# Kernel optimization log

Hardware: AMD Instinct MI355X
Metric: run time of the kernel (lower is better)

Reference implementation:

```python
import jax, jax.numpy as jnp
import numpy as np

B, S, HID = 16, 1024, 768
H, DH = 12, HID // 12


def setup_inputs() -> dict:
    key = jax.random.key(0)
    ks = jax.random.split(key, 10)
    scale = 1.0 / np.sqrt(HID)
    return {
        "hidden_states": jax.random.normal(ks[0], (B, S, HID), jnp.float32),
        "Wq": jax.random.normal(ks[1], (HID, HID), jnp.float32) * scale,
        "bq": jnp.zeros((HID,), jnp.float32),
        "Wk": jax.random.normal(ks[2], (HID, HID), jnp.float32) * scale,
        "bk": jnp.zeros((HID,), jnp.float32),
        "Wv": jax.random.normal(ks[3], (HID, HID), jnp.float32) * scale,
        "bv": jnp.zeros((HID,), jnp.float32),
        # torch init is zeros; use small randn so the linear-attention correction term is exercised
        "phi_k": jax.random.normal(ks[4], (1, H, DH, 1), jnp.float32) * 0.02,
        "phi_kv": jax.random.normal(ks[5], (1, H, DH, DH), jnp.float32) * 0.02,
    }


def _heads(x):
    # [B,S,HID] -> [B,H,S,DH]
    return x.reshape(B, S, H, DH).transpose(0, 2, 1, 3)


def reference(hidden_states, Wq, bq, Wk, bk, Wv, bv, phi_k, phi_kv):
    q = _heads(hidden_states @ Wq.T + bq)
    k = _heads(hidden_states @ Wk.T + bk)
    v = _heads(hidden_states @ Wv.T + bv)

    # phi(x) = ELU(x / d^0.25) + 1   (dropout disabled: eval-mode reference)
    phi_q = jax.nn.elu(q / jnp.asarray(DH, jnp.float32) ** 0.25) + 1.0

    # full softmax-style attention scores with max-subtract
    A = jnp.einsum("bhsd,bhtd->bhst", q, k) / jnp.sqrt(jnp.asarray(DH, jnp.float32))
    max_A = jnp.max(A, axis=-1, keepdims=True)          # [B,H,S,1]
    exp_max_A = jnp.exp(max_A)
    A = jnp.exp(A - max_A)                              # [B,H,S,S]

    # custom normalizer: softmax mass + linear-attention correction
    D = jnp.sum(A, axis=-1, keepdims=True) + jnp.matmul(phi_q, jnp.abs(phi_k)) / exp_max_A

    ctx = (jnp.matmul(A, v) + jnp.matmul(phi_q, phi_kv) / exp_max_A) / D  # [B,H,S,DH]
    out = ctx.transpose(0, 2, 1, 3).reshape(B, S, HID)
    return out
```

## Files before the change

### kernel.cpp

```cpp
#include <hip/hip_runtime.h>
#include <cstdint>
#include <cstddef>

typedef _Float16 f16x8 __attribute__((ext_vector_type(8)));
typedef _Float16 f16x4 __attribute__((ext_vector_type(4)));
typedef float    f32x4 __attribute__((ext_vector_type(4)));
typedef unsigned u32;
typedef const u32 __attribute__((address_space(1)))* gas_ptr;
typedef u32 __attribute__((address_space(3)))* las_ptr;

#define MFMA16(a, b, c) __builtin_amdgcn_mfma_f32_16x16x32_f16((a), (b), (c), 0, 0, 0)

static constexpr int Bb   = 16;
static constexpr int Ss   = 1024;
static constexpr int HID  = 768;
static constexpr int Hh   = 12;
static constexpr int DH   = 64;
static constexpr int Mrows = Bb * Ss;
static constexpr int N3    = 3 * HID;

static constexpr float QSCL  = 0.125f * 1.44269504088896f;
static constexpr float PHSCL = 1.9605161f;

__global__ void prep(const float* __restrict__ hs, _Float16* __restrict__ A16,
                     const float* __restrict__ Wq, const float* __restrict__ Wk,
                     const float* __restrict__ Wv, const float* __restrict__ bq,
                     const float* __restrict__ bk, const float* __restrict__ bv,
                     _Float16* __restrict__ Wt, float* __restrict__ bias) {
    const int i = blockIdx.x * 256 + threadIdx.x;
    if (i < Mrows * HID / 4) {
        float4 v = ((const float4*)hs)[i];
        f16x4 o;
        o[0] = (_Float16)v.x; o[1] = (_Float16)v.y;
        o[2] = (_Float16)v.z; o[3] = (_Float16)v.w;
        ((f16x4*)A16)[i] = o;
    }
    if (i < N3 * HID / 8) {
        const int i8 = i * 8;
        int n = i8 / HID;
        int k = i8 - n * HID;
        int sel = n / HID;
        int nn  = n - sel * HID;
        const float* W = (sel == 0) ? Wq : (sel == 1) ? Wk : Wv;
        const float* wp = W + (size_t)nn * HID + k;
        float4 v0 = *(const float4*)wp;
        float4 v1 = *(const float4*)(wp + 4);
        uint4 o;
        o.x = __builtin_bit_cast(u32, __builtin_amdgcn_cvt_pkrtz(v0.x, v0.y));
        o.y = __builtin_bit_cast(u32, __builtin_amdgcn_cvt_pkrtz(v0.z, v0.w));
        o.z = __builtin_bit_cast(u32, __builtin_amdgcn_cvt_pkrtz(v1.x, v1.y));
        o.w = __builtin_bit_cast(u32, __builtin_amdgcn_cvt_pkrtz(v1.z, v1.w));
        *(uint4*)(Wt + i8) = o;
    }
    if (i < N3) {
        int wsel = i / HID, j = i - wsel * HID;
        bias[i] = (wsel == 0) ? bq[j] : (wsel == 1) ? bk[j] : bv[j];
    }
}

__global__ __launch_bounds__(256, 2) void qkv_gemm(
    const _Float16* __restrict__ A, const _Float16* __restrict__ Bt,
    const float* __restrict__ bias,
    _Float16* __restrict__ Qo, _Float16* __restrict__ Ko, _Float16* __restrict__ VTo) {
    __shared__ _Float16 As[2][128 * 32];
    __shared__ _Float16 Bs[2][128 * 32];
    const int tid  = threadIdx.x;
    const int lane = tid & 63, wid = tid >> 6;
    const int g = lane >> 4, c = lane & 15;
    const int bm = blockIdx.x & 127, bn = blockIdx.x >> 7;
    const int m0 = bm * 128, n0 = bn * 128;
    const int wm = wid >> 1, wn = wid & 1;

    f32x4 acc[4][4] = {};

    auto stage = [&](int bf, int kt) {
#pragma unroll
        for (int i = 0; i < 2; ++i) {
            int ch  = i * 256 + wid * 64 + lane;
            int row = ch >> 2;
            int kh  = ((ch & 3) ^ ((row >> 1) & 3)) << 3;
            __builtin_amdgcn_global_load_lds(
                (gas_ptr)(A + (size_t)(m0 + row) * HID + kt + kh),
                (las_ptr)(&As[bf][(i * 256 + wid * 64) * 8]), 16, 0, 0);
            __builtin_amdgcn_global_load_lds(
                (gas_ptr)(Bt + (size_t)(n0 + row) * HID + kt + kh),
                (las_ptr)(&Bs[bf][(i * 256 + wid * 64) * 8]), 16, 0, 0);
        }
    };

    stage(0, 0);
    __syncthreads();

    for (int kt = 0; kt < HID; kt += 32) {
        const int cur = (kt >> 5) & 1;
        if (kt + 32 < HID) stage(cur ^ 1, kt + 32);

        f16x8 af[4], bf[4];
#pragma unroll
        for (int mi = 0; mi < 4; ++mi) {
            const int row = wm * 64 + mi * 16 + c;
            af[mi] = *(const f16x8*)((const char*)&As[cur][0] + row * 64 + ((g ^ ((row >> 1) & 3)) << 4));
        }
#pragma unroll
        for (int ni = 0; ni < 4; ++ni) {
            const int row = wn * 64 + ni * 16 + c;
            bf[ni] = *(const f16x8*)((const char*)&Bs[cur][0] + row * 64 + ((g ^ ((row >> 1) & 3)) << 4));
        }
#pragma unroll
        for (int mi = 0; mi < 4; ++mi)
#pragma unroll
            for (int ni = 0; ni < 4; ++ni)
                acc[mi][ni] = MFMA16(af[mi], bf[ni], acc[mi][ni]);

        __syncthreads();
    }

#pragma unroll
    for (int ni = 0; ni < 4; ++ni) {
        const int col    = n0 + wn * 64 + ni * 16 + c;
        const int which  = col / HID;
        const int within = col - which * HID;
        const int hh = within >> 6, d = within & 63;
        const float bias_v = bias[col];
        const float scl = (which == 0) ? QSCL : 1.0f;
#pragma unroll
        for (int mi = 0; mi < 4; ++mi) {
            const int rowg0 = m0 + wm * 64 + mi * 16 + g * 4;
            const int bidx = rowg0 >> 10, s0 = rowg0 & 1023;
            const int bh   = bidx * Hh + hh;
            f16x4 hv4;
#pragma unroll
            for (int r = 0; r < 4; ++r)
                hv4[r] = (_Float16)((acc[mi][ni][r] + bias_v) * scl);
            if (which == 2) {
                const int base64 = (m0 + wm * 64) & 1023;
                const int p = 32 * (mi >> 1) + 8 * g + 4 * (mi & 1);
                *(uint2*)(VTo + ((size_t)bh * DH + d) * Ss + base64 + p) = __builtin_bit_cast(uint2, hv4);
            } else if (which == 0) {
#pragma unroll
                for (int r = 0; r < 4; ++r)
                    Qo[((size_t)bh * Ss + s0 + r) * DH + d] = hv4[r];
            } else {
#pragma unroll
                for (int r = 0; r < 4; ++r)
                    Ko[((size_t)bh * Ss + s0 + r) * DH + d] = hv4[r];
            }
        }
    }
}

__global__ __launch_bounds__(256) void attn_kernel(
    const _Float16* __restrict__ Q, const _Float16* __restrict__ K,
    const _Float16* __restrict__ VT, const float* __restrict__ phi_k,
    const float* __restrict__ phi_kv, float* __restrict__ out) {
    __shared__ _Float16 Kb[2][64 * 64];
    __shared__ _Float16 Vb[2][64 * 64];

    const int tid  = threadIdx.x;
    const int lane = tid & 63, w = tid >> 6;
    const int g = lane >> 4, c = lane & 15;

    const int wg = (blockIdx.x & 7) * 192 + (blockIdx.x >> 3);
    const int bh = wg >> 3, qt = wg & 7;
    const int b = bh / Hh, h = bh - b * Hh;
    const size_t base = (size_t)bh * Ss * DH;
    const _Float16* Kg = K + base;
    const _Float16* Vg = VT + base;

    const int srow = lane >> 3;
    const int scol = (((lane & 7) ^ srow) << 4) >> 1;
    const int sw = (c & 7) << 4;

    const _Float16* Qp = Q + base + (size_t)(qt * 128 + w * 32 + c) * DH + g * 8;
    f16x8 aq[2][2];
    aq[0][0] = *(const f16x8*)(Qp);
    aq[0][1] = *(const f16x8*)(Qp + 32);
    aq[1][0] = *(const f16x8*)(Qp + 16 * DH);
    aq[1][1] = *(const f16x8*)(Qp + 16 * DH + 32);

    float part[2] = {0.f, 0.f};
    f32x4 acco[2][4] = {};

    auto stage = [&](int bf, int t0) {
#pragma unroll
        for (int i = 0; i < 2; ++i) {
            const int row0 = w * 16 + i * 8;
            __builtin_amdgcn_global_load_lds(
                (gas_ptr)(Kg + (size_t)(t0 + row0 + srow) * DH + scol),
                (las_ptr)(&Kb[bf][row0 * 64]), 16, 0, 0);
            __builtin_amdgcn_global_load_lds(
                (gas_ptr)(Vg + (size_t)(row0 + srow) * Ss + t0 + scol),
                (las_ptr)(&Vb[bf][row0 * 64]), 16, 0, 0);
        }
    };

    stage(0, 0);
    __syncthreads();

    for (int t0 = 0; t0 < Ss; t0 += 64) {
        const int bf = (t0 >> 6) & 1;
        if (t0 + 64 < Ss) stage(bf ^ 1, t0 + 64);

        f32x4 z[2][4];
        __builtin_amdgcn_s_setprio(1);
#pragma unroll
        for (int nt = 0; nt < 4; ++nt) {
            const char* kb = (const char*)&Kb[bf][0] + (nt * 16 + c) * 128;
            f16x8 bk0 = *(const f16x8*)(kb + ((g * 16) ^ sw));
            f16x8 bk1 = *(const f16x8*)(kb + ((64 + g * 16) ^ sw));
            f32x4 z0 = {}, z1 = {};
            z0 = MFMA16(bk0, aq[0][0], z0);
            z0 = MFMA16(bk1, aq[0][1], z0);
            z1 = MFMA16(bk0, aq[1][0], z1);
            z1 = MFMA16(bk1, aq[1][1], z1);
            z[0][nt] = z0;
            z[1][nt] = z1;
        }
        __builtin_amdgcn_s_setprio(0);

        f16x8 pb[2][2];
#pragma unroll
        for (int mb = 0; mb < 2; ++mb) {
#pragma unroll
            for (int kk = 0; kk < 2; ++kk) {
                float e0 = __builtin_amdgcn_exp2f(z[mb][2 * kk][0]);
                float e1 = __builtin_amdgcn_exp2f(z[mb][2 * kk][1]);
                float e2 = __builtin_amdgcn_exp2f(z[mb][2 * kk][2]);
                float e3 = __builtin_amdgcn_exp2f(z[mb][2 * kk][3]);
                float e4 = __builtin_amdgcn_exp2f(z[mb][2 * kk + 1][0]);
                float e5 = __builtin_amdgcn_exp2f(z[mb][2 * kk + 1][1]);
                float e6 = __builtin_amdgcn_exp2f(z[mb][2 * kk + 1][2]);
                float e7 = __builtin_amdgcn_exp2f(z[mb][2 * kk + 1][3]);
                part[mb] += (e0 + e1 + e2 + e3) + (e4 + e5 + e6 + e7);
                uint4 pk;
                pk.x = __builtin_bit_cast(u32, __builtin_amdgcn_cvt_pkrtz(e0, e1));
                pk.y = __builtin_bit_cast(u32, __builtin_amdgcn_cvt_pkrtz(e2, e3));
                pk.z = __builtin_bit_cast(u32, __builtin_amdgcn_cvt_pkrtz(e4, e5));
                pk.w = __builtin_bit_cast(u32, __builtin_amdgcn_cvt_pkrtz(e6, e7));
                pb[mb][kk] = __builtin_bit_cast(f16x8, pk);
            }
        }

        __builtin_amdgcn_s_setprio(1);
#pragma unroll
        for (int nd = 0; nd < 4; ++nd) {
            const char* vb = (const char*)&Vb[bf][0] + (nd * 16 + c) * 128;
#pragma unroll
            for (int kk = 0; kk < 2; ++kk) {
                f16x8 va = *(const f16x8*)(vb + ((kk * 64 + g * 16) ^ sw));
                acco[0][nd] = MFMA16(va, pb[0][kk], acco[0][nd]);
                acco[1][nd] = MFMA16(va, pb[1][kk], acco[1][nd]);
            }
        }
        __builtin_amdgcn_s_setprio(0);
        __syncthreads();
    }

    const float* phk = phi_k + h * DH;
    const float* pkv = phi_kv + h * DH * DH;

    f16x8 pq2[2][2];
    float invD[2];
#pragma unroll
    for (int mb = 0; mb < 2; ++mb) {
        const _Float16* Qr = Q + base + (size_t)(qt * 128 + w * 32 + mb * 16 + c) * DH;
        float dot = 0.f;
#pragma unroll
        for (int kk = 0; kk < 2; ++kk) {
            f16x4 qa = *(const f16x4*)(Qr + kk * 32 + 4 * g);
            f16x4 qb = *(const f16x4*)(Qr + kk * 32 + 16 + 4 * g);
            float4 fka = *(const float4*)(phk + kk * 32 + 4 * g);
            float4 fkb = *(const float4*)(phk + kk * 32 + 16 + 4 * g);
            const float fa[4] = {fka.x, fka.y, fka.z, fka.w};
            const float fb[4] = {fkb.x, fkb.y, fkb.z, fkb.w};
            f16x8 pq;
#pragma unroll
            for (int j = 0; j < 4; ++j) {
                float x0 = (float)qa[j] * PHSCL;
                float x1 = (float)qb[j] * PHSCL;
                float p0 = (x0 > 0.f) ? (x0 + 1.f) : __expf(x0);
                float p1 = (x1 > 0.f) ? (x1 + 1.f) : __expf(x1);
                dot += p0 * fabsf(fa[j]) + p1 * fabsf(fb[j]);
                pq[j]     = (_Float16)p0;
                pq[4 + j] = (_Float16)p1;
            }
            pq2[mb][kk] = pq;
        }
        dot += __shfl_xor(dot, 16);
        dot += __shfl_xor(dot, 32);
        float s = part[mb];
        s += __shfl_xor(s, 16);
        s += __shfl_xor(s, 32);
        invD[mb] = 1.f / (s + dot);
    }

#pragma unroll
    for (int nd = 0; nd < 4; ++nd) {
        f16x8 fa[2];
#pragma unroll
        for (int kk = 0; kk < 2; ++kk) {
            f16x8 t;
#pragma unroll
            for (int j = 0; j < 8; ++j) {
                int dh = kk * 32 + 16 * (j >> 2) + 4 * g + (j & 3);
                t[j] = (_Float16)pkv[dh * DH + nd * 16 + c];
            }
            fa[kk] = t;
        }
#pragma unroll
        for (int mb = 0; mb < 2; ++mb) {
            f32x4 cc = {};
            cc = MFMA16(fa[0], pq2[mb][0], cc);
            cc = MFMA16(fa[1], pq2[mb][1], cc);
            f32x4 o = (acco[mb][nd] + cc) * invD[mb];
            const int srow_o = qt * 128 + w * 32 + mb * 16 + c;
            float* op = out + ((size_t)b * Ss + srow_o) * HID + h * DH + nd * 16 + 4 * g;
            *(f32x4*)op = o;
        }
    }
}

extern "C" void kernel_launch(void* const* d_in, const int* in_sizes, int n_in,
                              void* d_out, int out_size, void* d_ws, size_t ws_size,
                              hipStream_t stream) {
    (void)in_sizes; (void)n_in; (void)out_size;
    const float* hs   = (const float*)d_in[0];
    const float* Wq   = (const float*)d_in[1];
    const float* bq   = (const float*)d_in[2];
    const float* Wk   = (const float*)d_in[3];
    const float* bk   = (const float*)d_in[4];
    const float* Wv   = (const float*)d_in[5];
    const float* bv   = (const float*)d_in[6];
    const float* phik = (const float*)d_in[7];
    const float* phikv= (const float*)d_in[8];
    float* out = (float*)d_out;

    char* ws = (char*)d_ws;
    constexpr size_t szA   = (size_t)Mrows * HID * 2;
    constexpr size_t szWt  = (size_t)N3 * HID * 2;
    constexpr size_t szBia = (size_t)N3 * 4;
    constexpr size_t szQ   = (size_t)Bb * Hh * Ss * DH * 2;
    _Float16* A16  = (_Float16*)(ws);
    _Float16* Wt   = (_Float16*)(ws + szA);
    float*    bias = (float*)(ws + szA + szWt);
    _Float16* Qb   = (_Float16*)(ws + szA + szWt + szBia);
    _Float16* Kb   = (_Float16*)(ws + szA + szWt + szBia + szQ);
    _Float16* VTb  = (_Float16*)(ws + szA + szWt + szBia + 2 * szQ);
    (void)ws_size;

    prep<<<(Mrows * HID / 4 + 255) / 256, 256, 0, stream>>>(hs, A16, Wq, Wk, Wv, bq, bk, bv, Wt, bias);
    qkv_gemm<<<dim3((Mrows / 128) * (N3 / 128)), 256, 0, stream>>>(A16, Wt, bias, Qb, Kb, VTb);
    attn_kernel<<<dim3(Bb * Hh * (Ss / 128)), 256, 0, stream>>>(Qb, Kb, VTb, phik, phikv, out);
}
```

Baseline: 178.2 us.

## Replace double-buffered K=32 QKV GEMM staging with single-buffer K=64 tiles

```diff
diff --git a/kernel.cpp b/kernel.cpp
--- a/kernel.cpp
+++ b/kernel.cpp
@@ -62,8 +62,8 @@
     const _Float16* __restrict__ A, const _Float16* __restrict__ Bt,
     const float* __restrict__ bias,
     _Float16* __restrict__ Qo, _Float16* __restrict__ Ko, _Float16* __restrict__ VTo) {
-    __shared__ _Float16 As[2][128 * 32];
-    __shared__ _Float16 Bs[2][128 * 32];
+    __shared__ _Float16 As[128 * 64];
+    __shared__ _Float16 Bs[128 * 64];
     const int tid  = threadIdx.x;
     const int lane = tid & 63, wid = tid >> 6;
     const int g = lane >> 4, c = lane & 15;
@@ -71,48 +71,44 @@
     const int m0 = bm * 128, n0 = bn * 128;
     const int wm = wid >> 1, wn = wid & 1;
 
+    const int srk = ((lane & 7) ^ (lane >> 3)) << 3;
+
     f32x4 acc[4][4] = {};
 
-    auto stage = [&](int bf, int kt) {
-#pragma unroll
-        for (int i = 0; i < 2; ++i) {
-            int ch  = i * 256 + wid * 64 + lane;
-            int row = ch >> 2;
-            int kh  = ((ch & 3) ^ ((row >> 1) & 3)) << 3;
+    for (int kt = 0; kt < HID; kt += 64) {
+        if (kt) __syncthreads();
+#pragma unroll
+        for (int i = 0; i < 4; ++i) {
+            const int ch  = i * 256 + wid * 64 + lane;
+            const int row = ch >> 3;
             __builtin_amdgcn_global_load_lds(
-                (gas_ptr)(A + (size_t)(m0 + row) * HID + kt + kh),
-                (las_ptr)(&As[bf][(i * 256 + wid * 64) * 8]), 16, 0, 0);
+                (gas_ptr)(A + (size_t)(m0 + row) * HID + kt + srk),
+                (las_ptr)(As + (i * 256 + wid * 64) * 8), 16, 0, 0);
             __builtin_amdgcn_global_load_lds(
-                (gas_ptr)(Bt + (size_t)(n0 + row) * HID + kt + kh),
-                (las_ptr)(&Bs[bf][(i * 256 + wid * 64) * 8]), 16, 0, 0);
-        }
-    };
-
-    stage(0, 0);
-    __syncthreads();
-
-    for (int kt = 0; kt < HID; kt += 32) {
-        const int cur = (kt >> 5) & 1;
-        if (kt + 32 < HID) stage(cur ^ 1, kt + 32);
-
-        f16x8 af[4], bf[4];
-#pragma unroll
-        for (int mi = 0; mi < 4; ++mi) {
-            const int row = wm * 64 + mi * 16 + c;
-            af[mi] = *(const f16x8*)((const char*)&As[cur][0] + row * 64 + ((g ^ ((row >> 1) & 3)) << 4));
-        }
-#pragma unroll
-        for (int ni = 0; ni < 4; ++ni) {
-            const int row = wn * 64 + ni * 16 + c;
-            bf[ni] = *(const f16x8*)((const char*)&Bs[cur][0] + row * 64 + ((g ^ ((row >> 1) & 3)) << 4));
-        }
-#pragma unroll
-        for (int mi = 0; mi < 4; ++mi)
-#pragma unroll
-            for (int ni = 0; ni < 4; ++ni)
-                acc[mi][ni] = MFMA16(af[mi], bf[ni], acc[mi][ni]);
-
+                (gas_ptr)(Bt + (size_t)(n0 + row) * HID + kt + srk),
+                (las_ptr)(Bs + (i * 256 + wid * 64) * 8), 16, 0, 0);
+        }
         __syncthreads();
+
+#pragma unroll
+        for (int kk = 0; kk < 2; ++kk) {
+            f16x8 af[4], bf[4];
+#pragma unroll
+            for (int mi = 0; mi < 4; ++mi) {
+                const int row = wm * 64 + mi * 16 + c;
+                af[mi] = *(const f16x8*)((const char*)As + row * 128 + ((((kk * 4 + g) ^ (c & 7))) << 4));
+            }
+#pragma unroll
+            for (int ni = 0; ni < 4; ++ni) {
+                const int row = wn * 64 + ni * 16 + c;
+                bf[ni] = *(const f16x8*)((const char*)Bs + row * 128 + ((((kk * 4 + g) ^ (c & 7))) << 4));
+            }
+#pragma unroll
+            for (int mi = 0; mi < 4; ++mi)
+#pragma unroll
+                for (int ni = 0; ni < 4; ++ni)
+                    acc[mi][ni] = MFMA16(af[mi], bf[ni], acc[mi][ni]);
+        }
     }
 
 #pragma unroll
```

Measured after the change: 174.4 us. 1.02x faster.
